# Kernel tuning notes

Hardware: AMD Instinct MI355X
Metric: run time of the kernel (lower is better)

## Reference

```python
import jax, jax.numpy as jnp
import numpy as np

N = 50000      # num_nodes
E = 800000     # num_edges
H = 64         # hidden_dim
L = 4          # num_layers
NH = 4         # num_heads
HD = H // NH   # head_dim


def setup_inputs() -> dict:
    key = jax.random.key(0)
    ks = iter(jax.random.split(key, 64))
    def nrm(shape, s=0.1):
        return jax.random.normal(next(ks), shape, jnp.float32) * s
    inp = dict(
        x=jax.random.normal(next(ks), (N, 4), jnp.float32),
        edge_index=jax.random.randint(next(ks), (2, E), 0, N),
        edge_attr=jax.random.normal(next(ks), (E, 2), jnp.float32),
        in_w=nrm((4, H)), in_b=jnp.zeros((H,), jnp.float32),
        conv_rw1=nrm((L, H + 2, H)), conv_rb1=jnp.zeros((L, H), jnp.float32),
        conv_rw2=nrm((L, H, H)), conv_rb2=jnp.zeros((L, H), jnp.float32),
        conv_iw1=nrm((L, H + 2, H)), conv_ib1=jnp.zeros((L, H), jnp.float32),
        conv_iw2=nrm((L, H, H)), conv_ib2=jnp.zeros((L, H), jnp.float32),
        conv_sw=nrm((L, H, 4 * H)), conv_sb=jnp.zeros((L, 4 * H), jnp.float32),
        att_qw=nrm((L, 4, H)), att_qb=jnp.zeros((L, H), jnp.float32),
        att_kw=nrm((L, 4, H)), att_kb=jnp.zeros((L, H), jnp.float32),
        att_vw=nrm((L, 4, H)), att_vb=jnp.zeros((L, H), jnp.float32),
        att_ow=nrm((L, H, 4)), att_ob=jnp.zeros((L, 4), jnp.float32),
        ln_g=jnp.ones((L, 4), jnp.float32), ln_b=jnp.zeros((L, 4), jnp.float32),
        out_w1=nrm((H, H // 2)), out_b1=jnp.zeros((H // 2,), jnp.float32),
        out_w2=nrm((H // 2, 4)), out_b2=jnp.zeros((4,), jnp.float32),
        res_w=jnp.full((L,), 0.1, jnp.float32),
    )
    return inp


def reference(x, edge_index, edge_attr, in_w, in_b,
              conv_rw1, conv_rb1, conv_rw2, conv_rb2,
              conv_iw1, conv_ib1, conv_iw2, conv_ib2,
              conv_sw, conv_sb,
              att_qw, att_qb, att_kw, att_kb, att_vw, att_vb, att_ow, att_ob,
              ln_g, ln_b, out_w1, out_b1, out_w2, out_b2, res_w):
    n = x.shape[0]
    row, col = edge_index[0], edge_index[1]
    # add_self_loops with edge_attr fill 0 (used only inside the conv)
    loops = jnp.arange(n)
    row_sl = jnp.concatenate([row, loops])
    col_sl = jnp.concatenate([col, loops])
    ea_sl = jnp.concatenate([edge_attr, jnp.zeros((n, 2), edge_attr.dtype)], axis=0)
    deg = jax.ops.segment_sum(jnp.ones((row_sl.shape[0],), x.dtype), col_sl,
                              num_segments=n)[:, None]  # >=1 due to self loops

    h = x @ in_w + in_b  # [N, H]
    for i in range(L):
        residual = x
        # ---- ComplexGraphConv (mean aggregation, source_to_target) ----
        msg_in = jnp.concatenate([h[row_sl], ea_sl], axis=-1)  # [E+N, H+2]
        real = jax.nn.relu(msg_in @ conv_rw1[i] + conv_rb1[i]) @ conv_rw2[i] + conv_rb2[i]
        imag = jax.nn.relu(msg_in @ conv_iw1[i] + conv_ib1[i]) @ conv_iw2[i] + conv_ib2[i]
        mag = jnp.sqrt(real * real + imag * imag)
        phase = jnp.arctan2(imag, real + 1e-8)
        msg = jnp.concatenate([real, imag, mag, phase], axis=-1)  # [E+N, 4H]
        agg = jax.ops.segment_sum(msg, col_sl, num_segments=n) / deg
        h4 = agg + (h @ conv_sw[i] + conv_sb[i])  # [N, 4H]
        x4 = h4[:, :4]
        # ---- ComplexGraphAttention (global edge softmax per head) ----
        Q = (x4 @ att_qw[i] + att_qb[i]).reshape(n, NH, HD)
        K = (x4 @ att_kw[i] + att_kb[i]).reshape(n, NH, HD)
        V = (x4 @ att_vw[i] + att_vb[i]).reshape(n, NH, HD)
        scores = jnp.einsum('ehd,ehd->eh', Q[row], K[col]) / np.sqrt(HD).astype(x.dtype)
        w = jax.nn.softmax(scores, axis=0)  # softmax over ALL edges (dim=0)
        att = jax.ops.segment_sum(w[:, :, None] * V[row], col,
                                  num_segments=n).reshape(n, NH * HD)
        x4 = (att @ att_ow[i] + att_ob[i]) + x4  # out_proj + residual (dropout=eval)
        # ---- LayerNorm over last dim (4) ----
        mu = x4.mean(-1, keepdims=True)
        var = x4.var(-1, keepdims=True)
        x4 = (x4 - mu) / jnp.sqrt(var + 1e-5) * ln_g[i] + ln_b[i]
        x = x4 + residual * res_w[i]
        h = x @ in_w + in_b
    pred = jnp.tanh(jax.nn.relu(h @ out_w1 + out_b1) @ out_w2 + out_b2) * 0.3
    return pred
```

## Files before the change

kernel.cpp:

```cpp
#include <hip/hip_runtime.h>
#include <hip/hip_bf16.h>
#include <hip/hip_fp16.h>

#define N_NODES 50000
#define N_EDGES 800000
#define BUCKET 64
#define EDGE_TB 3125
#define COPY_NB 196

__device__ __forceinline__ float rdlane(float v, int k) {
    return __uint_as_float(__builtin_amdgcn_readlane(__float_as_uint(v), k));
}
template <int CTRL>
__device__ __forceinline__ float dpp_addf(float v) {
    int x = __builtin_amdgcn_update_dpp(0, __float_as_int(v), CTRL, 0xF, 0xF, true);
    return v + __int_as_float(x);
}
#define DPP_QX1  0xB1
#define DPP_QX2  0x4E
#define DPP_HM   0x141
#define DPP_RM   0x140
#define DPP_ROR4 0x124
#define DPP_ROR8 0x128
__device__ __forceinline__ float dpp_sum16(float v) {
    v = dpp_addf<DPP_QX1>(v);
    v = dpp_addf<DPP_QX2>(v);
    v = dpp_addf<DPP_HM>(v);
    v = dpp_addf<DPP_RM>(v);
    return v;
}
__device__ __forceinline__ void bsum4(float& v0, float& v1, float& v2, float& v3) {
    #pragma unroll
    for (int m = 1; m < 64; m <<= 1) {
        v0 += __shfl_xor(v0, m);
        v1 += __shfl_xor(v1, m);
        v2 += __shfl_xor(v2, m);
        v3 += __shfl_xor(v3, m);
    }
}

__global__ void k_setup(const float* __restrict__ x, unsigned* __restrict__ cntC,
                        float4* __restrict__ xcur,
                        const int* __restrict__ row, const int* __restrict__ col,
                        const float* __restrict__ ea, uint2* __restrict__ colEA,
                        const float* __restrict__ qw, const float* __restrict__ qb,
                        const float* __restrict__ kw, const float* __restrict__ kb,
                        const float* __restrict__ vw, const float* __restrict__ vb,
                        const float* __restrict__ ow,
                        const float* __restrict__ in_w, const float* __restrict__ in_b,
                        const float* __restrict__ rw1all, const float* __restrict__ rb1all,
                        const float* __restrict__ swall,
                        float* __restrict__ cst, float* __restrict__ cstV,
                        float* __restrict__ cstM) {
    int tid = threadIdx.x;
    int bid = blockIdx.x;
    if (bid < EDGE_TB) {
        int e = bid * 256 + tid;
        if (e < N_EDGES) {
            int c = col[e];
            unsigned slot = atomicAdd(&cntC[c], 1u);
            float2 e2 = ((const float2*)ea)[e];
            __half2 h2 = __floats2half2_rn(e2.x, e2.y);
            colEA[(size_t)c * BUCKET + slot] =
                make_uint2(*reinterpret_cast<unsigned*>(&h2), (unsigned)row[e]);
        }
        return;
    }
    if (bid < EDGE_TB + COPY_NB) {
        int n = (bid - EDGE_TB) * 256 + tid;
        if (n < N_NODES) xcur[n] = ((const float4*)x)[n];
        return;
    }
    int pb = bid - (EDGE_TB + COPY_NB);
    int m = tid;
    if (m >= 64) return;
    int d = m & 15;
    if (pb < 4) {
        int L = pb;
        const float* qwl = qw + L * 256; const float* kwl = kw + L * 256;
        const float* qbl = qb + L * 64;  const float* kbl = kb + L * 64;
        float qa[4], ka[4];
        #pragma unroll
        for (int a = 0; a < 4; a++) { qa[a] = qwl[a * 64 + m]; ka[a] = kwl[a * 64 + m]; }
        float qbm = qbl[m], kbm = kbl[m];
        float vals[25];
        int idx = 0;
        #pragma unroll
        for (int a = 0; a < 4; a++)
            #pragma unroll
            for (int b = 0; b < 4; b++) vals[idx++] = qa[a] * ka[b];
        #pragma unroll
        for (int a = 0; a < 4; a++) vals[idx++] = qa[a] * kbm;
        #pragma unroll
        for (int b = 0; b < 4; b++) vals[idx++] = qbm * ka[b];
        vals[24] = qbm * kbm;
        #pragma unroll
        for (int i = 0; i < 25; i++) {
            float v = vals[i];
            v += __shfl_xor(v, 1); v += __shfl_xor(v, 2);
            v += __shfl_xor(v, 4); v += __shfl_xor(v, 8);
            vals[i] = v;
        }
        if (d == 0) {
            float* out = cst + L * 128 + (m >> 4) * 32;
            #pragma unroll
            for (int i = 0; i < 25; i++) out[i] = vals[i] * 0.25f;
        }
    } else if (pb < 8) {
        int L = pb - 4;
        int h = m >> 4;
        const float* vwl = vw + L * 256;
        const float* vbl = vb + L * 64;
        float4 owv = ((const float4*)(ow + L * 256))[m];
        float vals[20];
        #pragma unroll
        for (int a = 0; a < 4; a++) {
            float v = vwl[a * 64 + m];
            vals[a * 4 + 0] = v * owv.x; vals[a * 4 + 1] = v * owv.y;
            vals[a * 4 + 2] = v * owv.z; vals[a * 4 + 3] = v * owv.w;
        }
        float b = vbl[m];
        vals[16] = b * owv.x; vals[17] = b * owv.y; vals[18] = b * owv.z; vals[19] = b * owv.w;
        #pragma unroll
        for (int i = 0; i < 20; i++) {
            float v = vals[i];
            v += __shfl_xor(v, 1); v += __shfl_xor(v, 2);
            v += __shfl_xor(v, 4); v += __shfl_xor(v, 8);
            vals[i] = v;
        }
        if (d == 0) {
            float* out = cstV + L * 128 + h * 32;
            #pragma unroll
            for (int i = 0; i < 20; i++) out[i] = vals[i];
        }
    } else {
        int L = pb - 8;
        const float* rw1 = rw1all + L * 66 * 64;
        const float* rb1 = rb1all + L * 64;
        const float* sw  = swall + L * 64 * 256;
        float* M = cstM + L * 384;
        float bacc = rb1[m];
        float w0 = 0.f, w1 = 0.f, w2 = 0.f, w3 = 0.f;
        for (int k = 0; k < 64; k++) {
            float r = rw1[k * 64 + m];
            bacc += in_b[k] * r;
            w0 += in_w[k] * r;
            w1 += in_w[64 + k] * r;
            w2 += in_w[128 + k] * r;
            w3 += in_w[192 + k] * r;
        }
        M[m * 4 + 0] = w0; M[m * 4 + 1] = w1; M[m * 4 + 2] = w2; M[m * 4 + 3] = w3;
        M[256 + m] = bacc;
        if (m < 16) {
            int a = m >> 2, o = m & 3;
            float sacc = 0.f;
            for (int k = 0; k < 64; k++) sacc += in_w[a * 64 + k] * sw[k * 256 + o];
            M[320 + m] = sacc;
        }
        if (m < 4) {
            float sacc = 0.f;
            for (int k = 0; k < 64; k++) sacc += in_b[k] * sw[k * 256 + m];
            M[336 + m] = sacc;
        }
    }
}

__global__ void k61(const float* __restrict__ att16, const float* __restrict__ sumexpP,
                    const float4* __restrict__ x4b, const float* __restrict__ ob,
                    const float* __restrict__ g, const float* __restrict__ bb,
                    const float* __restrict__ resw, float4* __restrict__ xcur) {
    int tid = threadIdx.x;
    int wid = (blockIdx.x * blockDim.x + tid) >> 6;
    int lane = tid & 63;
    int n0 = wid * 4;
    if (n0 >= N_NODES) return;
    float4 zp = ((const float4*)sumexpP)[lane];
    bsum4(zp.x, zp.y, zp.z, zp.w);
    int hh = (lane & 15) >> 2;
    float z = (hh == 0) ? zp.x : (hh == 1) ? zp.y : (hh == 2) ? zp.z : zp.w;
    float ob0 = ob[0], ob1 = ob[1], ob2 = ob[2], ob3 = ob[3];
    float g0 = g[0], g1 = g[1], g2 = g[2], g3 = g[3];
    float bb0 = bb[0], bb1 = bb[1], bb2 = bb[2], bb3 = bb[3];
    float rw = resw[0];
    #pragma unroll
    for (int i = 0; i < 4; i++) {
        int n = n0 + i;
        float a = 0.f;
        if (n < N_NODES && lane < 16) a = att16[n * 16 + lane] / z;
        a = dpp_addf<DPP_ROR4>(a);
        a = dpp_addf<DPP_ROR8>(a);
        float y0 = rdlane(a, 0), y1 = rdlane(a, 1), y2 = rdlane(a, 2), y3 = rdlane(a, 3);
        if (n < N_NODES) {
            float4 x4v = x4b[n];
            y0 += ob0 + x4v.x; y1 += ob1 + x4v.y;
            y2 += ob2 + x4v.z; y3 += ob3 + x4v.w;
            float mu = 0.25f * (y0 + y1 + y2 + y3);
            float d0 = y0 - mu, d1 = y1 - mu, d2 = y2 - mu, d3 = y3 - mu;
            float var = 0.25f * (d0 * d0 + d1 * d1 + d2 * d2 + d3 * d3);
            float rs = rsqrtf(var + 1e-5f);
            float4 xold = xcur[n];
            float nn0 = d0 * rs * g0 + bb0 + xold.x * rw;
            float nn1 = d1 * rs * g1 + bb1 + xold.y * rw;
            float nn2 = d2 * rs * g2 + bb2 + xold.z * rw;
            float nn3 = d3 * rs * g3 + bb3 + xold.w * rw;
            if (lane == 0) xcur[n] = make_float4(nn0, nn1, nn2, nn3);
        }
    }
}

__global__ void k23b(const unsigned* __restrict__ cntC, const uint2* __restrict__ colEA,
                     const float4* __restrict__ xcur, const float* __restrict__ rw1,
                     const float* __restrict__ rw2, const float* __restrict__ cstM,
                     const float* __restrict__ rb2, const float* __restrict__ sb,
                     float4* __restrict__ x4b, float* __restrict__ sumexpP) {
    __shared__ float4 s_weff4[64];
    __shared__ float4 s_bw1[64];
    __shared__ float4 s_rw24[64];
    __shared__ float  s_sw16[16];
    __shared__ float  s_sbe[4];
    int tid = threadIdx.x;
    if (tid < 64) {
        s_weff4[tid] = ((const float4*)cstM)[tid];
        s_bw1[tid]   = make_float4(cstM[256 + tid], rw1[4096 + tid], rw1[4160 + tid], 0.f);
        s_rw24[tid]  = *(const float4*)(rw2 + tid * 64);
    }
    if (tid < 16) s_sw16[tid] = cstM[320 + tid];
    if (tid < 4)  s_sbe[tid]  = cstM[336 + tid];
    if (blockIdx.x == 0) sumexpP[tid] = 0.f;
    __syncthreads();
    int l16 = tid & 15, grp = tid >> 4;
    int c = blockIdx.x * 16 + grp;
    float4 xc = xcur[c];
    int cnt = (int)cntC[c];
    const uint2* rowE = colEA + (size_t)c * BUCKET;
    int items = cnt + 1;
    float a0 = 0.f, a1 = 0.f, a2 = 0.f, a3 = 0.f;
    for (int base = 0; base < items; base += 16) {
        int it = base + l16;
        bool act = it < items;
        float4 xr = make_float4(0.f, 0.f, 0.f, 0.f);
        float exv = 0.f, eyv = 0.f;
        if (act) {
            if (it == 0) {
                xr = xc;
            } else {
                uint2 er = rowE[it - 1];
                xr = xcur[er.y];
                __half2 eh = *reinterpret_cast<const __half2*>(&er.x);
                float2 ef = __half22float2(eh);
                exv = ef.x; eyv = ef.y;
            }
        }
        float actf = act ? 1.f : 0.f;
        #pragma unroll 4
        for (int ch = 0; ch < 64; ch++) {
            float4 wv = s_weff4[ch];
            float4 bw = s_bw1[ch];
            float tk = bw.x + xr.x * wv.x + xr.y * wv.y + xr.z * wv.z + xr.w * wv.w;
            float pre = tk + exv * bw.y + eyv * bw.z;
            float rr = fmaxf(pre, 0.f) * actf;
            float4 r2 = s_rw24[ch];
            a0 += rr * r2.x; a1 += rr * r2.y; a2 += rr * r2.z; a3 += rr * r2.w;
        }
    }
    a0 = dpp_sum16(a0); a1 = dpp_sum16(a1); a2 = dpp_sum16(a2); a3 = dpp_sum16(a3);
    if (l16 == 0) {
        float idg = 1.f / (float)(cnt + 1);
        float b0 = xc.x * s_sw16[0] + xc.y * s_sw16[4] + xc.z * s_sw16[8]  + xc.w * s_sw16[12] + s_sbe[0];
        float b1 = xc.x * s_sw16[1] + xc.y * s_sw16[5] + xc.z * s_sw16[9]  + xc.w * s_sw16[13] + s_sbe[1];
        float b2 = xc.x * s_sw16[2] + xc.y * s_sw16[6] + xc.z * s_sw16[10] + xc.w * s_sw16[14] + s_sbe[2];
        float b3 = xc.x * s_sw16[3] + xc.y * s_sw16[7] + xc.z * s_sw16[11] + xc.w * s_sw16[15] + s_sbe[3];
        x4b[c] = make_float4(a0 * idg + b0 + rb2[0] + sb[0],
                             a1 * idg + b1 + rb2[1] + sb[1],
                             a2 * idg + b2 + rb2[2] + sb[2],
                             a3 * idg + b3 + rb2[3] + sb[3]);
    }
}

__global__ void k5_att(const unsigned* __restrict__ cntC, const uint2* __restrict__ colEA,
                       const float4* __restrict__ x4b, const float* __restrict__ cst,
                       const float* __restrict__ cstV, float* __restrict__ att16,
                       float* __restrict__ sumexpP) {
    __shared__ float s_cst[128];
    __shared__ float s_cstV[128];
    __shared__ float zs[16][4];
    int tid = threadIdx.x;
    if (tid < 128) { s_cst[tid] = cst[tid]; s_cstV[tid] = cstV[tid]; }
    __syncthreads();
    int l16 = tid & 15, grp = tid >> 4;
    int c = blockIdx.x * 16 + grp;
    float4 xc = x4b[c];
    float gh[4][4], bh[4];
    #pragma unroll
    for (int h = 0; h < 4; h++) {
        const float* C = s_cst + h * 32;
        gh[h][0] = xc.x * C[0]  + xc.y * C[1]  + xc.z * C[2]  + xc.w * C[3]  + C[16];
        gh[h][1] = xc.x * C[4]  + xc.y * C[5]  + xc.z * C[6]  + xc.w * C[7]  + C[17];
        gh[h][2] = xc.x * C[8]  + xc.y * C[9]  + xc.z * C[10] + xc.w * C[11] + C[18];
        gh[h][3] = xc.x * C[12] + xc.y * C[13] + xc.z * C[14] + xc.w * C[15] + C[19];
        bh[h]    = C[20] * xc.x + C[21] * xc.y + C[22] * xc.z + C[23] * xc.w + C[24];
    }
    int cnt = (int)cntC[c];
    const unsigned* rowY = (const unsigned*)(colEA + (size_t)c * BUCKET);
    float S00 = 0.f, S01 = 0.f, S02 = 0.f, S03 = 0.f;
    float S10 = 0.f, S11 = 0.f, S12 = 0.f, S13 = 0.f;
    float S20 = 0.f, S21 = 0.f, S22 = 0.f, S23 = 0.f;
    float S30 = 0.f, S31 = 0.f, S32 = 0.f, S33 = 0.f;
    float z0 = 0.f, z1 = 0.f, z2 = 0.f, z3 = 0.f;
    for (int base = 0; base < cnt; base += 16) {
        int it = base + l16;
        bool act = it < cnt;
        float4 xr = make_float4(0.f, 0.f, 0.f, 0.f);
        if (act) xr = x4b[rowY[2 * it + 1]];
        float actf = act ? 1.f : 0.f;
        {
            float s = xr.x * gh[0][0] + xr.y * gh[0][1] + xr.z * gh[0][2] + xr.w * gh[0][3] + bh[0];
            float ex = __expf(s) * actf;
            z0 += ex; S00 += ex * xr.x; S01 += ex * xr.y; S02 += ex * xr.z; S03 += ex * xr.w;
        }
        {
            float s = xr.x * gh[1][0] + xr.y * gh[1][1] + xr.z * gh[1][2] + xr.w * gh[1][3] + bh[1];
            float ex = __expf(s) * actf;
            z1 += ex; S10 += ex * xr.x; S11 += ex * xr.y; S12 += ex * xr.z; S13 += ex * xr.w;
        }
        {
            float s = xr.x * gh[2][0] + xr.y * gh[2][1] + xr.z * gh[2][2] + xr.w * gh[2][3] + bh[2];
            float ex = __expf(s) * actf;
            z2 += ex; S20 += ex * xr.x; S21 += ex * xr.y; S22 += ex * xr.z; S23 += ex * xr.w;
        }
        {
            float s = xr.x * gh[3][0] + xr.y * gh[3][1] + xr.z * gh[3][2] + xr.w * gh[3][3] + bh[3];
            float ex = __expf(s) * actf;
            z3 += ex; S30 += ex * xr.x; S31 += ex * xr.y; S32 += ex * xr.z; S33 += ex * xr.w;
        }
    }
    S00 = dpp_sum16(S00); S01 = dpp_sum16(S01); S02 = dpp_sum16(S02); S03 = dpp_sum16(S03);
    S10 = dpp_sum16(S10); S11 = dpp_sum16(S11); S12 = dpp_sum16(S12); S13 = dpp_sum16(S13);
    S20 = dpp_sum16(S20); S21 = dpp_sum16(S21); S22 = dpp_sum16(S22); S23 = dpp_sum16(S23);
    S30 = dpp_sum16(S30); S31 = dpp_sum16(S31); S32 = dpp_sum16(S32); S33 = dpp_sum16(S33);
    z0 = dpp_sum16(z0); z1 = dpp_sum16(z1); z2 = dpp_sum16(z2); z3 = dpp_sum16(z3);
    int h = l16 >> 2, a = l16 & 3;
    float Sa0 = (h == 0) ? S00 : (h == 1) ? S10 : (h == 2) ? S20 : S30;
    float Sa1 = (h == 0) ? S01 : (h == 1) ? S11 : (h == 2) ? S21 : S31;
    float Sa2 = (h == 0) ? S02 : (h == 1) ? S12 : (h == 2) ? S22 : S32;
    float Sa3 = (h == 0) ? S03 : (h == 1) ? S13 : (h == 2) ? S23 : S33;
    float zh  = (h == 0) ? z0  : (h == 1) ? z1  : (h == 2) ? z2  : z3;
    const float* V = s_cstV + h * 32;
    float my = Sa0 * V[0 * 4 + a] + Sa1 * V[1 * 4 + a] + Sa2 * V[2 * 4 + a] + Sa3 * V[3 * 4 + a]
             + zh * V[16 + a];
    att16[c * 16 + l16] = my;
    if (a == 0) zs[grp][h] = zh;
    __syncthreads();
    if (tid < 4) {
        float acc = 0.f;
        #pragma unroll
        for (int q = 0; q < 16; q++) acc += zs[q][tid];
        atomicAdd(&sumexpP[((blockIdx.x & 63) << 2) + tid], acc);
    }
}

__global__ void k6pred(const float* __restrict__ att16, const float* __restrict__ sumexpP,
                       const float4* __restrict__ x4b, const float* __restrict__ ob,
                       const float* __restrict__ g, const float* __restrict__ bb,
                       const float* __restrict__ resw, const float4* __restrict__ xcur,
                       const float* __restrict__ in_w, const float* __restrict__ in_b,
                       const float* __restrict__ w1, const float* __restrict__ b1,
                       const float* __restrict__ w2, const float* __restrict__ b2,
                       float* __restrict__ out) {
    int tid = threadIdx.x;
    int node = (blockIdx.x * blockDim.x + tid) >> 6;
    int lane = tid & 63;
    if (node >= N_NODES) return;
    float4 zp = ((const float4*)sumexpP)[lane];
    bsum4(zp.x, zp.y, zp.z, zp.w);
    int hh = (lane & 15) >> 2;
    float z = (hh == 0) ? zp.x : (hh == 1) ? zp.y : (hh == 2) ? zp.z : zp.w;
    float a = 0.f;
    if (lane < 16) a = att16[node * 16 + lane] / z;
    a = dpp_addf<DPP_ROR4>(a);
    a = dpp_addf<DPP_ROR8>(a);
    float y0 = rdlane(a, 0), y1 = rdlane(a, 1), y2 = rdlane(a, 2), y3 = rdlane(a, 3);
    float4 x4v = x4b[node];
    y0 += ob[0] + x4v.x; y1 += ob[1] + x4v.y;
    y2 += ob[2] + x4v.z; y3 += ob[3] + x4v.w;
    float mu = 0.25f * (y0 + y1 + y2 + y3);
    float d0 = y0 - mu, d1 = y1 - mu, d2 = y2 - mu, d3 = y3 - mu;
    float var = 0.25f * (d0 * d0 + d1 * d1 + d2 * d2 + d3 * d3);
    float rs = rsqrtf(var + 1e-5f);
    float4 xold = xcur[node];
    float rw = resw[0];
    float n0 = d0 * rs * g[0] + bb[0] + xold.x * rw;
    float n1 = d1 * rs * g[1] + bb[1] + xold.y * rw;
    float n2 = d2 * rs * g[2] + bb[2] + xold.z * rw;
    float n3 = d3 * rs * g[3] + bb[3] + xold.w * rw;
    float hv = in_b[lane] + n0 * in_w[lane] + n1 * in_w[64 + lane]
             + n2 * in_w[128 + lane] + n3 * in_w[192 + lane];
    int j2 = lane & 31;
    float m = b1[j2];
    for (int k = 0; k < 64; k++) m += rdlane(hv, k) * w1[k * 32 + j2];
    m = fmaxf(m, 0.f);
    float4 w2v = ((const float4*)w2)[j2];
    float v0 = m * w2v.x, v1 = m * w2v.y, v2 = m * w2v.z, v3 = m * w2v.w;
    bsum4(v0, v1, v2, v3);
    float o0 = tanhf(0.5f * v0 + b2[0]) * 0.3f;
    float o1 = tanhf(0.5f * v1 + b2[1]) * 0.3f;
    float o2 = tanhf(0.5f * v2 + b2[2]) * 0.3f;
    float o3 = tanhf(0.5f * v3 + b2[3]) * 0.3f;
    if (lane == 0) ((float4*)out)[node] = make_float4(o0, o1, o2, o3);
}

extern "C" void kernel_launch(void* const* d_in, const int* in_sizes, int n_in,
                              void* d_out, int out_size, void* d_ws, size_t ws_size,
                              hipStream_t stream) {
    const float* x        = (const float*)d_in[0];
    const int*   ei       = (const int*)d_in[1];
    const float* ea       = (const float*)d_in[2];
    const float* in_w     = (const float*)d_in[3];
    const float* in_b     = (const float*)d_in[4];
    const float* conv_rw1 = (const float*)d_in[5];
    const float* conv_rb1 = (const float*)d_in[6];
    const float* conv_rw2 = (const float*)d_in[7];
    const float* conv_rb2 = (const float*)d_in[8];
    const float* conv_sw  = (const float*)d_in[13];
    const float* conv_sb  = (const float*)d_in[14];
    const float* att_qw   = (const float*)d_in[15];
    const float* att_qb   = (const float*)d_in[16];
    const float* att_kw   = (const float*)d_in[17];
    const float* att_kb   = (const float*)d_in[18];
    const float* att_vw   = (const float*)d_in[19];
    const float* att_vb   = (const float*)d_in[20];
    const float* att_ow   = (const float*)d_in[21];
    const float* att_ob   = (const float*)d_in[22];
    const float* ln_g     = (const float*)d_in[23];
    const float* ln_b     = (const float*)d_in[24];
    const float* out_w1   = (const float*)d_in[25];
    const float* out_b1   = (const float*)d_in[26];
    const float* out_w2   = (const float*)d_in[27];
    const float* out_b2   = (const float*)d_in[28];
    const float* res_w    = (const float*)d_in[29];

    const int* row = ei;
    const int* col = ei + N_EDGES;

    char* ws = (char*)d_ws;
    size_t off = 0;
    auto alloc = [&](size_t bytes) -> void* {
        void* p = ws + off;
        off = (off + bytes + 255) & ~(size_t)255;
        return p;
    };
    unsigned* cntC     = (unsigned*)alloc(N_NODES * 4);
    uint2*    colEA    = (uint2*)alloc((size_t)N_NODES * BUCKET * 8);
    float*    att16    = (float*)alloc((size_t)N_NODES * 16 * 4);
    float4*   x4b      = (float4*)alloc((size_t)N_NODES * 16);
    float4*   xcur     = (float4*)alloc((size_t)N_NODES * 16);
    float*    cst      = (float*)alloc(4 * 128 * 4);
    float*    cstV     = (float*)alloc(4 * 128 * 4);
    float*    cstM     = (float*)alloc(4 * 384 * 4);
    float*    sumexpP  = (float*)alloc(64 * 4 * 4);

    dim3 b256(256);
    int grpBlocks   = (N_NODES + 15) / 16;
    int nodeBlocks4 = (N_NODES + 15) / 16;

    hipMemsetAsync(cntC, 0, N_NODES * 4, stream);
    k_setup<<<EDGE_TB + COPY_NB + 12, b256, 0, stream>>>(
        x, cntC, xcur, row, col, ea, colEA,
        att_qw, att_qb, att_kw, att_kb, att_vw, att_vb, att_ow,
        in_w, in_b, conv_rw1, conv_rb1, conv_sw,
        cst, cstV, cstM);

    for (int i = 0; i < 4; i++) {
        const float* rw1 = conv_rw1 + i * 66 * 64;
        const float* rw2 = conv_rw2 + i * 64 * 64;
        const float* rb2 = conv_rb2 + i * 64;
        const float* sbl = conv_sb + i * 256;

        if (i > 0) {
            k61<<<nodeBlocks4, b256, 0, stream>>>(att16, sumexpP, x4b,
                                                  att_ob + (i - 1) * 4, ln_g + (i - 1) * 4,
                                                  ln_b + (i - 1) * 4, res_w + (i - 1),
                                                  xcur);
        }
        k23b<<<grpBlocks, b256, 0, stream>>>(cntC, colEA, xcur, rw1, rw2,
                                             cstM + i * 384, rb2, sbl, x4b, sumexpP);
        k5_att<<<grpBlocks, b256, 0, stream>>>(cntC, colEA, x4b, cst + i * 128,
                                               cstV + i * 128, att16, sumexpP);
    }
    k6pred<<<(N_NODES + 3) / 4, b256, 0, stream>>>(att16, sumexpP, x4b, att_ob + 12, ln_g + 12,
                                            ln_b + 12, res_w + 3, xcur, in_w, in_b,
                                            out_w1, out_b1, out_w2, out_b2, (float*)d_out);
}
```

Before: 496.7 us.

## Repartition k23b so each lane owns four channels with register-resident weights

The per-node message MLP in k23b used to assign one edge per lane and loop over all 64 channels, reading weights from shared memory every iteration. It now stages the group's edge inputs in shared memory, and each of the 16 lanes owns 4 channels whose weights are held in registers, looping only over the active edges. This removes the per-channel LDS weight reads and the wasted work on inactive padded edges, replacing them with broadcast LDS reads of edge data. It relies on the 16-lane group staying in one wavefront without a barrier, and it adds register pressure.

After: 407.7 us. 1.22x faster.

```diff
diff --git a/kernel.cpp b/kernel.cpp
--- a/kernel.cpp
+++ b/kernel.cpp
@@ -213,22 +213,35 @@
                      const float* __restrict__ rw2, const float* __restrict__ cstM,
                      const float* __restrict__ rb2, const float* __restrict__ sb,
                      float4* __restrict__ x4b, float* __restrict__ sumexpP) {
-    __shared__ float4 s_weff4[64];
-    __shared__ float4 s_bw1[64];
-    __shared__ float4 s_rw24[64];
-    __shared__ float  s_sw16[16];
-    __shared__ float  s_sbe[4];
+    __shared__ float s_rw2[64][4];
+    __shared__ float s_weff[64][4];
+    __shared__ float s_w1[128];
+    __shared__ float s_beff[64];
+    __shared__ float s_sw16[16];
+    __shared__ float s_sbe[4];
+    __shared__ float4 s_x[16][16];
+    __shared__ float2 s_e[16][16];
     int tid = threadIdx.x;
-    if (tid < 64) {
-        s_weff4[tid] = ((const float4*)cstM)[tid];
-        s_bw1[tid]   = make_float4(cstM[256 + tid], rw1[4096 + tid], rw1[4160 + tid], 0.f);
-        s_rw24[tid]  = *(const float4*)(rw2 + tid * 64);
-    }
+    { int r = tid >> 2, cc = tid & 3; s_rw2[r][cc] = rw2[r * 64 + cc]; s_weff[r][cc] = cstM[tid]; }
+    if (tid < 128) s_w1[tid] = rw1[64 * 64 + tid];
+    if (tid < 64) s_beff[tid] = cstM[256 + tid];
     if (tid < 16) s_sw16[tid] = cstM[320 + tid];
     if (tid < 4)  s_sbe[tid]  = cstM[336 + tid];
     if (blockIdx.x == 0) sumexpP[tid] = 0.f;
     __syncthreads();
     int l16 = tid & 15, grp = tid >> 4;
+    float wf[4][4], bfr[4], w1a[4], w1b[4], wr2r[4][4];
+    #pragma unroll
+    for (int j = 0; j < 4; j++) {
+        int ch = l16 * 4 + j;
+        #pragma unroll
+        for (int a = 0; a < 4; a++) wf[j][a] = s_weff[ch][a];
+        bfr[j] = s_beff[ch];
+        w1a[j] = s_w1[ch];
+        w1b[j] = s_w1[64 + ch];
+        #pragma unroll
+        for (int o = 0; o < 4; o++) wr2r[j][o] = s_rw2[ch][o];
+    }
     int c = blockIdx.x * 16 + grp;
     float4 xc = xcur[c];
     int cnt = (int)cntC[c];
@@ -237,30 +250,33 @@
     float a0 = 0.f, a1 = 0.f, a2 = 0.f, a3 = 0.f;
     for (int base = 0; base < items; base += 16) {
         int it = base + l16;
-        bool act = it < items;
         float4 xr = make_float4(0.f, 0.f, 0.f, 0.f);
-        float exv = 0.f, eyv = 0.f;
-        if (act) {
+        float2 ef2 = make_float2(0.f, 0.f);
+        if (it < items) {
             if (it == 0) {
                 xr = xc;
             } else {
                 uint2 er = rowE[it - 1];
                 xr = xcur[er.y];
                 __half2 eh = *reinterpret_cast<const __half2*>(&er.x);
-                float2 ef = __half22float2(eh);
-                exv = ef.x; eyv = ef.y;
+                ef2 = __half22float2(eh);
             }
         }
-        float actf = act ? 1.f : 0.f;
-        #pragma unroll 4
-        for (int ch = 0; ch < 64; ch++) {
-            float4 wv = s_weff4[ch];
-            float4 bw = s_bw1[ch];
-            float tk = bw.x + xr.x * wv.x + xr.y * wv.y + xr.z * wv.z + xr.w * wv.w;
-            float pre = tk + exv * bw.y + eyv * bw.z;
-            float rr = fmaxf(pre, 0.f) * actf;
-            float4 r2 = s_rw24[ch];
-            a0 += rr * r2.x; a1 += rr * r2.y; a2 += rr * r2.z; a3 += rr * r2.w;
+        s_x[grp][l16] = xr;
+        s_e[grp][l16] = ef2;
+        int lim = items - base; if (lim > 16) lim = 16;
+        for (int q = 0; q < lim; q++) {
+            float4 xq = s_x[grp][q];
+            float2 eq = s_e[grp][q];
+            #pragma unroll
+            for (int j = 0; j < 4; j++) {
+                float tk = bfr[j] + xq.x * wf[j][0] + xq.y * wf[j][1]
+                         + xq.z * wf[j][2] + xq.w * wf[j][3];
+                float pre = tk + eq.x * w1a[j] + eq.y * w1b[j];
+                float rr = fmaxf(pre, 0.f);
+                a0 += rr * wr2r[j][0]; a1 += rr * wr2r[j][1];
+                a2 += rr * wr2r[j][2]; a3 += rr * wr2r[j][3];
+            }
         }
     }
     a0 = dpp_sum16(a0); a1 = dpp_sum16(a1); a2 = dpp_sum16(a2); a3 = dpp_sum16(a3);
```
